# Performance work log

Hardware: AMD Instinct MI355X
Metric: run time of the kernel (lower is better)

## Reference

```python
import jax, jax.numpy as jnp
import numpy as np

B, T, C, H = 2, 512, 64, 64  # batch, seq (<= block_size), n_embd, head_size


def setup_inputs() -> dict:
    key = jax.random.key(0)
    ks = jax.random.split(key, 9)
    p = lambda k, sh: jax.random.normal(k, sh, jnp.float32) * 0.02
    return {
        "x": jax.random.normal(ks[0], (B, T, C), jnp.float32),
        "pos_emb": jax.random.normal(ks[1], (T, C), jnp.float32),
        "pos_dist_emb": jax.random.normal(ks[2], (B, T, T, 2 * C), jnp.float32),
        # GeluFeedForward(4c -> c -> 1): Linear(4c, c) -> GELU -> Linear(c, 1)
        "W1": p(ks[3], (4 * C, C)),
        "b1": p(ks[4], (C,)),
        "W2": p(ks[5], (C, 1)),
        "b2": p(ks[6], (1,)),
        # value projection Linear(c, head_size)
        "Wv": p(ks[7], (C, H)),
        "bv": p(ks[8], (H,)),
    }


def reference(x, pos_emb, pos_dist_emb, W1, b1, W2, b2, Wv, bv):
    b, t, c = x.shape
    x1 = x + pos_emb  # (b,t,c)
    # cat([k, q, pos_dist], -1) @ W1 == k@W1[:c] + q@W1[c:2c] + pd@W1[2c:]
    # (avoids materializing the (b,t,t,4c) repeat+cat tensor; same math)
    W1k, W1q, W1p = W1[:c], W1[c:2 * c], W1[2 * c:]
    kp = x1 @ W1k                 # (b,t,c): key side, varies over pair axis 2
    qp = x1 @ W1q                 # (b,t,c): query side, varies over pair axis 1
    pp = pos_dist_emb @ W1p       # (b,t,t,c)
    h = jax.nn.gelu(qp[:, :, None, :] + kp[:, None, :, :] + pp + b1,
                    approximate=False)          # (b,t,t,c)
    wei = ((h @ W2)[..., 0] + b2[0]) * (c ** -0.5)  # (b,t,t)
    causal = jnp.tril(jnp.ones((t, t), bool))
    wei = jnp.where(causal, wei, -jnp.inf)
    wei = jax.nn.softmax(wei, axis=-1)          # (b,t,t); dropout p=0
    v = x @ Wv + bv                             # (b,t,H)
    return wei @ v                              # (b,t,H)
```

## Files before the change

### kernel.cpp

```cpp
#include <hip/hip_runtime.h>
#include <math.h>

#define BB 2
#define TT 512
#define CC 64
#define HH 64
#define KK 128
#define PADK 136
#define JT 64

typedef __attribute__((ext_vector_type(8))) short short8;
typedef __attribute__((ext_vector_type(4))) float float4v;

__device__ inline unsigned short f2bf(float f) {
    unsigned int u = __float_as_uint(f);
    u = (u + 0x7FFFu + ((u >> 16) & 1u)) >> 16;
    return (unsigned short)u;
}

__global__ __launch_bounds__(256) void pack_kernel(
    const float* __restrict__ W1, unsigned short* __restrict__ Wpt)
{
    int t = blockIdx.x * 256 + threadIdx.x;
    int c = t >> 7;
    int k = t & 127;
    Wpt[c * PADK + k] = f2bf(W1[(2 * CC + k) * CC + c]);
}

__global__ __launch_bounds__(64) void prep_kernel(
    const float* __restrict__ x, const float* __restrict__ pos_emb,
    const float* __restrict__ W1, const float* __restrict__ b1,
    const float* __restrict__ Wv, const float* __restrict__ bv,
    float* __restrict__ kp, float* __restrict__ qpb, float* __restrict__ v)
{
    const int row = blockIdx.x;
    const int t = row & (TT - 1);
    const int c = threadIdx.x;
    __shared__ float xs[CC], x1s[CC];
    float xv = x[row * CC + c];
    xs[c] = xv;
    x1s[c] = xv + pos_emb[t * CC + c];
    __syncthreads();
    float ak = 0.f, aq = 0.f, av = 0.f;
#pragma unroll 8
    for (int k = 0; k < CC; ++k) {
        ak = fmaf(x1s[k], W1[k * CC + c], ak);
        aq = fmaf(x1s[k], W1[(CC + k) * CC + c], aq);
        av = fmaf(xs[k], Wv[k * HH + c], av);
    }
    kp[row * CC + c] = ak;
    qpb[row * CC + c] = aq + b1[c];
    v[row * HH + c] = av + bv[c];
}

__global__ __launch_bounds__(256) void wei_kernel(
    const float* __restrict__ pd, const unsigned short* __restrict__ Wpt,
    const float* __restrict__ W2, const float* __restrict__ b2,
    const float* __restrict__ kp, const float* __restrict__ qpb,
    float* __restrict__ wei)
{
    const int i = blockIdx.y;
    const int b = blockIdx.z;
    const int j0 = blockIdx.x * JT;
    if (j0 > i) return;

    __shared__ unsigned short Alds[JT * PADK];
    __shared__ unsigned short Blds[CC * PADK];

    const int tid = threadIdx.x;

    {
        const uint4* __restrict__ src = (const uint4*)Wpt;
        uint4* dst = (uint4*)Blds;
#pragma unroll
        for (int f = 0; f < 5; ++f) {
            int idx = f * 256 + tid;
            if (idx < (CC * PADK) / 8) dst[idx] = src[idx];
        }
    }

    {
        const float4* __restrict__ p4 =
            (const float4*)(pd + (((size_t)b * TT + i) * TT + j0) * KK);
#pragma unroll
        for (int it = 0; it < 8; ++it) {
            int f = it * 256 + tid;
            float4 val = p4[f];
            int j = f >> 5;
            int kq = f & 31;
            uint2 u;
            u.x = (unsigned)f2bf(val.x) | ((unsigned)f2bf(val.y) << 16);
            u.y = (unsigned)f2bf(val.z) | ((unsigned)f2bf(val.w) << 16);
            *(uint2*)&Alds[j * PADK + kq * 4] = u;
        }
    }
    __syncthreads();

    const int wave = tid >> 6;
    const int lane = tid & 63;
    const int m = lane & 15;
    const int kg = lane >> 4;

    float4v acc[4] = {{0.f,0.f,0.f,0.f},{0.f,0.f,0.f,0.f},
                      {0.f,0.f,0.f,0.f},{0.f,0.f,0.f,0.f}};
    const int arow = wave * 16 + m;
#pragma unroll
    for (int kt = 0; kt < 4; ++kt) {
        short8 a = *(const short8*)&Alds[arow * PADK + kt * 32 + kg * 8];
#pragma unroll
        for (int nt = 0; nt < 4; ++nt) {
            short8 bf = *(const short8*)&Blds[(nt * 16 + m) * PADK + kt * 32 + kg * 8];
            acc[nt] = __builtin_amdgcn_mfma_f32_16x16x32_bf16(a, bf, acc[nt], 0, 0, 0);
        }
    }

    float w2v[4], qv[4];
#pragma unroll
    for (int nt = 0; nt < 4; ++nt) {
        int c = nt * 16 + m;
        w2v[nt] = W2[c];
        qv[nt] = qpb[((size_t)b * TT + i) * CC + c];
    }
    const float b2v = b2[0];

#pragma unroll
    for (int r = 0; r < 4; ++r) {
        const int j = j0 + wave * 16 + kg * 4 + r;
        float s = 0.f;
#pragma unroll
        for (int nt = 0; nt < 4; ++nt) {
            float tv = acc[nt][r] + qv[nt] + kp[((size_t)b * TT + j) * CC + nt * 16 + m];
            float g = 0.5f * tv * (1.f + erff(tv * 0.70710678118654752f));
            s = fmaf(g, w2v[nt], s);
        }
#pragma unroll
        for (int off = 1; off < 16; off <<= 1) s += __shfl_xor(s, off);
        if (m == r && j <= i)
            wei[((size_t)b * TT + i) * TT + j] = (s + b2v) * 0.125f;
    }
}

__device__ inline float wave_reduce_max(float m) {
#pragma unroll
    for (int off = 32; off > 0; off >>= 1) m = fmaxf(m, __shfl_down(m, off));
    return m;
}
__device__ inline float wave_reduce_sum(float s) {
#pragma unroll
    for (int off = 32; off > 0; off >>= 1) s += __shfl_down(s, off);
    return s;
}

__global__ __launch_bounds__(256) void out_kernel(
    const float* __restrict__ wei, const float* __restrict__ v,
    float* __restrict__ out)
{
    const int i = blockIdx.x;
    const int b = blockIdx.y;
    const int tid = threadIdx.x;
    const int wv = tid >> 6;
    const int lane = tid & 63;
    const int n = i + 1;

    __shared__ float p[TT];
    __shared__ float red[4];
    __shared__ float part[4][HH];

    float m = -1e30f;
    for (int jj = tid; jj < n; jj += 256) {
        float w = wei[((size_t)b * TT + i) * TT + jj];
        p[jj] = w;
        m = fmaxf(m, w);
    }
    m = wave_reduce_max(m);
    if (lane == 0) red[wv] = m;
    __syncthreads();
    const float M = fmaxf(fmaxf(red[0], red[1]), fmaxf(red[2], red[3]));
    __syncthreads();

    float s = 0.f;
    for (int jj = tid; jj < n; jj += 256) {
        float e = __expf(p[jj] - M);
        p[jj] = e;
        s += e;
    }
    s = wave_reduce_sum(s);
    if (lane == 0) red[wv] = s;
    __syncthreads();
    const float S = red[0] + red[1] + red[2] + red[3];
    const float inv = 1.f / S;

    float acc = 0.f, acc2 = 0.f;
    int jj = wv;
    for (; jj + 4 < n; jj += 8) {
        acc  = fmaf(p[jj],     v[((size_t)b * TT + jj) * HH + lane], acc);
        acc2 = fmaf(p[jj + 4], v[((size_t)b * TT + jj + 4) * HH + lane], acc2);
    }
    if (jj < n)
        acc = fmaf(p[jj], v[((size_t)b * TT + jj) * HH + lane], acc);
    acc += acc2;
    part[wv][lane] = acc;
    __syncthreads();
    if (tid < HH) {
        float r = (part[0][tid] + part[1][tid] + part[2][tid] + part[3][tid]) * inv;
        out[((size_t)b * TT + i) * HH + tid] = r;
    }
}

extern "C" void kernel_launch(void* const* d_in, const int* in_sizes, int n_in,
                              void* d_out, int out_size, void* d_ws, size_t ws_size,
                              hipStream_t stream)
{
    const float* x       = (const float*)d_in[0];
    const float* pos_emb = (const float*)d_in[1];
    const float* pd      = (const float*)d_in[2];
    const float* W1      = (const float*)d_in[3];
    const float* b1      = (const float*)d_in[4];
    const float* W2      = (const float*)d_in[5];
    const float* b2      = (const float*)d_in[6];
    const float* Wv      = (const float*)d_in[7];
    const float* bv      = (const float*)d_in[8];
    float* out = (float*)d_out;

    float* ws = (float*)d_ws;
    unsigned short* Wpt = (unsigned short*)ws;
    float* kp  = ws + 4608;
    float* qpb = ws + 4608 + 65536;
    float* v   = ws + 4608 + 131072;
    float* wei = ws + 4608 + 196608;

    pack_kernel<<<dim3(32), dim3(256), 0, stream>>>(W1, Wpt);
    prep_kernel<<<dim3(BB * TT), dim3(64), 0, stream>>>(x, pos_emb, W1, b1, Wv, bv, kp, qpb, v);
    wei_kernel<<<dim3(TT / JT, TT, BB), dim3(256), 0, stream>>>(pd, Wpt, W2, b2, kp, qpb, wei);
    out_kernel<<<dim3(TT, BB), dim3(256), 0, stream>>>(wei, v, out);
}
```

Before: 405.4 us.

## Hold W1 fragments in registers, swizzle LDS, fuse weight packing into prep

The bf16 W1 slice is pre-packed in MFMA fragment order by extra blocks of prep_kernel, which removes the separate pack launch. wei_kernel then loads the B fragments directly into registers instead of staging them in LDS. This roughly halves shared memory per block, and launch bounds now request higher occupancy. The A tile drops its padding in favour of an XOR swizzle, kp values are prefetched before the barrier, and out_kernel accumulates with float4 loads and shuffle reductions. The trade-off is more register pressure from 16 short8 fragments plus kv values, which could cause spills under the tighter launch bounds.

```diff
diff --git a/kernel.cpp b/kernel.cpp
--- a/kernel.cpp
+++ b/kernel.cpp
@@ -6,7 +6,6 @@
 #define CC 64
 #define HH 64
 #define KK 128
-#define PADK 136
 #define JT 64
 
 typedef __attribute__((ext_vector_type(8))) short short8;
@@ -18,21 +17,30 @@
     return (unsigned short)u;
 }
 
-__global__ __launch_bounds__(256) void pack_kernel(
-    const float* __restrict__ W1, unsigned short* __restrict__ Wpt)
-{
-    int t = blockIdx.x * 256 + threadIdx.x;
-    int c = t >> 7;
-    int k = t & 127;
-    Wpt[c * PADK + k] = f2bf(W1[(2 * CC + k) * CC + c]);
-}
-
 __global__ __launch_bounds__(64) void prep_kernel(
     const float* __restrict__ x, const float* __restrict__ pos_emb,
     const float* __restrict__ W1, const float* __restrict__ b1,
     const float* __restrict__ Wv, const float* __restrict__ bv,
-    float* __restrict__ kp, float* __restrict__ qpb, float* __restrict__ v)
-{
+    float* __restrict__ kp, float* __restrict__ qpb, float* __restrict__ v,
+    unsigned short* __restrict__ Wpt)
+{
+    if (blockIdx.x >= BB * TT) {
+        int base = (blockIdx.x - BB * TT) * 256 + threadIdx.x;
+#pragma unroll
+        for (int q = 0; q < 4; ++q) {
+            int o  = base + q * 64;
+            int e  = o & 7;
+            int mm = (o >> 3) & 15;
+            int kg = (o >> 7) & 3;
+            int kt = (o >> 9) & 3;
+            int nt = (o >> 11) & 3;
+            int k = kt * 32 + kg * 8 + e;
+            int c = nt * 16 + mm;
+            Wpt[o] = f2bf(W1[(2 * CC + k) * CC + c]);
+        }
+        return;
+    }
+
     const int row = blockIdx.x;
     const int t = row & (TT - 1);
     const int c = threadIdx.x;
@@ -53,7 +61,7 @@
     v[row * HH + c] = av + bv[c];
 }
 
-__global__ __launch_bounds__(256) void wei_kernel(
+__global__ __launch_bounds__(256, 8) void wei_kernel(
     const float* __restrict__ pd, const unsigned short* __restrict__ Wpt,
     const float* __restrict__ W2, const float* __restrict__ b2,
     const float* __restrict__ kp, const float* __restrict__ qpb,
@@ -64,20 +72,36 @@
     const int j0 = blockIdx.x * JT;
     if (j0 > i) return;
 
-    __shared__ unsigned short Alds[JT * PADK];
-    __shared__ unsigned short Blds[CC * PADK];
-
-    const int tid = threadIdx.x;
-
-    {
-        const uint4* __restrict__ src = (const uint4*)Wpt;
-        uint4* dst = (uint4*)Blds;
-#pragma unroll
-        for (int f = 0; f < 5; ++f) {
-            int idx = f * 256 + tid;
-            if (idx < (CC * PADK) / 8) dst[idx] = src[idx];
-        }
-    }
+    __shared__ unsigned short Alds[JT * KK];
+
+    const int tid  = threadIdx.x;
+    const int wave = tid >> 6;
+    const int lane = tid & 63;
+    const int m    = lane & 15;
+    const int kg   = lane >> 4;
+
+    short8 bfrag[4][4];
+#pragma unroll
+    for (int nt = 0; nt < 4; ++nt)
+#pragma unroll
+        for (int kt = 0; kt < 4; ++kt)
+            bfrag[nt][kt] = *(const short8*)&Wpt[((nt * 4 + kt) * 64 + lane) * 8];
+
+    float w2v[4], qv[4], kv[4][4];
+#pragma unroll
+    for (int nt = 0; nt < 4; ++nt) {
+        int c = nt * 16 + m;
+        w2v[nt] = W2[c];
+        qv[nt]  = qpb[((size_t)b * TT + i) * CC + c];
+    }
+#pragma unroll
+    for (int r = 0; r < 4; ++r) {
+        int j = j0 + wave * 16 + kg * 4 + r;
+#pragma unroll
+        for (int nt = 0; nt < 4; ++nt)
+            kv[r][nt] = kp[((size_t)b * TT + j) * CC + nt * 16 + m];
+    }
+    const float b2v = b2[0];
 
     {
         const float4* __restrict__ p4 =
@@ -86,42 +110,28 @@
         for (int it = 0; it < 8; ++it) {
             int f = it * 256 + tid;
             float4 val = p4[f];
-            int j = f >> 5;
+            int j  = f >> 5;
             int kq = f & 31;
             uint2 u;
             u.x = (unsigned)f2bf(val.x) | ((unsigned)f2bf(val.y) << 16);
             u.y = (unsigned)f2bf(val.z) | ((unsigned)f2bf(val.w) << 16);
-            *(uint2*)&Alds[j * PADK + kq * 4] = u;
+            *(uint2*)&Alds[j * KK + ((kq * 4) ^ ((j & 7) << 3))] = u;
         }
     }
     __syncthreads();
-
-    const int wave = tid >> 6;
-    const int lane = tid & 63;
-    const int m = lane & 15;
-    const int kg = lane >> 4;
 
     float4v acc[4] = {{0.f,0.f,0.f,0.f},{0.f,0.f,0.f,0.f},
                       {0.f,0.f,0.f,0.f},{0.f,0.f,0.f,0.f}};
-    const int arow = wave * 16 + m;
+    const int arow  = wave * 16 + m;
+    const int abase = arow * KK;
+    const int a7    = (arow & 7) << 3;
 #pragma unroll
     for (int kt = 0; kt < 4; ++kt) {
-        short8 a = *(const short8*)&Alds[arow * PADK + kt * 32 + kg * 8];
-#pragma unroll
-        for (int nt = 0; nt < 4; ++nt) {
-            short8 bf = *(const short8*)&Blds[(nt * 16 + m) * PADK + kt * 32 + kg * 8];
-            acc[nt] = __builtin_amdgcn_mfma_f32_16x16x32_bf16(a, bf, acc[nt], 0, 0, 0);
-        }
-    }
-
-    float w2v[4], qv[4];
-#pragma unroll
-    for (int nt = 0; nt < 4; ++nt) {
-        int c = nt * 16 + m;
-        w2v[nt] = W2[c];
-        qv[nt] = qpb[((size_t)b * TT + i) * CC + c];
-    }
-    const float b2v = b2[0];
+        short8 a = *(const short8*)&Alds[abase + ((kt * 32 + kg * 8) ^ a7)];
+#pragma unroll
+        for (int nt = 0; nt < 4; ++nt)
+            acc[nt] = __builtin_amdgcn_mfma_f32_16x16x32_bf16(a, bfrag[nt][kt], acc[nt], 0, 0, 0);
+    }
 
 #pragma unroll
     for (int r = 0; r < 4; ++r) {
@@ -129,7 +139,7 @@
         float s = 0.f;
 #pragma unroll
         for (int nt = 0; nt < 4; ++nt) {
-            float tv = acc[nt][r] + qv[nt] + kp[((size_t)b * TT + j) * CC + nt * 16 + m];
+            float tv = acc[nt][r] + qv[nt] + kv[r][nt];
             float g = 0.5f * tv * (1.f + erff(tv * 0.70710678118654752f));
             s = fmaf(g, w2v[nt], s);
         }
@@ -164,16 +174,18 @@
 
     __shared__ float p[TT];
     __shared__ float red[4];
-    __shared__ float part[4][HH];
-
-    float m = -1e30f;
+    __shared__ float4v part[4][16];
+
+    const float* wrow = wei + ((size_t)b * TT + i) * TT;
+
+    float mx = -1e30f;
     for (int jj = tid; jj < n; jj += 256) {
-        float w = wei[((size_t)b * TT + i) * TT + jj];
+        float w = wrow[jj];
         p[jj] = w;
-        m = fmaxf(m, w);
-    }
-    m = wave_reduce_max(m);
-    if (lane == 0) red[wv] = m;
+        mx = fmaxf(mx, w);
+    }
+    mx = wave_reduce_max(mx);
+    if (lane == 0) red[wv] = mx;
     __syncthreads();
     const float M = fmaxf(fmaxf(red[0], red[1]), fmaxf(red[2], red[3]));
     __syncthreads();
@@ -190,20 +202,31 @@
     const float S = red[0] + red[1] + red[2] + red[3];
     const float inv = 1.f / S;
 
-    float acc = 0.f, acc2 = 0.f;
-    int jj = wv;
-    for (; jj + 4 < n; jj += 8) {
-        acc  = fmaf(p[jj],     v[((size_t)b * TT + jj) * HH + lane], acc);
-        acc2 = fmaf(p[jj + 4], v[((size_t)b * TT + jj + 4) * HH + lane], acc2);
-    }
-    if (jj < n)
-        acc = fmaf(p[jj], v[((size_t)b * TT + jj) * HH + lane], acc);
-    acc += acc2;
-    part[wv][lane] = acc;
-    __syncthreads();
-    if (tid < HH) {
-        float r = (part[0][tid] + part[1][tid] + part[2][tid] + part[3][tid]) * inv;
-        out[((size_t)b * TT + i) * HH + tid] = r;
+    const int c4 = lane & 15;
+    const int jr = lane >> 4;
+    const float4v* v4 = (const float4v*)(v + (size_t)b * TT * HH);
+    float4v acc = {0.f, 0.f, 0.f, 0.f};
+    for (int base = wv * 4; base < n; base += 16) {
+        int j = base + jr;
+        float pj = (j < n) ? p[j] : 0.f;
+        int jc = (j < n) ? j : 0;
+        float4v vv = v4[jc * 16 + c4];
+        acc += vv * pj;
+    }
+#pragma unroll
+    for (int off = 16; off <= 32; off <<= 1) {
+        float4v t;
+        t[0] = __shfl_xor(acc[0], off);
+        t[1] = __shfl_xor(acc[1], off);
+        t[2] = __shfl_xor(acc[2], off);
+        t[3] = __shfl_xor(acc[3], off);
+        acc += t;
+    }
+    if (jr == 0) part[wv][c4] = acc;
+    __syncthreads();
+    if (tid < 16) {
+        float4v r = (part[0][tid] + part[1][tid] + part[2][tid] + part[3][tid]) * inv;
+        *((float4v*)(out + ((size_t)b * TT + i) * HH) + tid) = r;
     }
 }
 
@@ -224,13 +247,12 @@
 
     float* ws = (float*)d_ws;
     unsigned short* Wpt = (unsigned short*)ws;
-    float* kp  = ws + 4608;
-    float* qpb = ws + 4608 + 65536;
-    float* v   = ws + 4608 + 131072;
-    float* wei = ws + 4608 + 196608;
-
-    pack_kernel<<<dim3(32), dim3(256), 0, stream>>>(W1, Wpt);
-    prep_kernel<<<dim3(BB * TT), dim3(64), 0, stream>>>(x, pos_emb, W1, b1, Wv, bv, kp, qpb, v);
+    float* kp  = ws + 4096;
+    float* qpb = ws + 4096 + 65536;
+    float* v   = ws + 4096 + 131072;
+    float* wei = ws + 4096 + 196608;
+
+    prep_kernel<<<dim3(BB * TT + 32), dim3(64), 0, stream>>>(x, pos_emb, W1, b1, Wv, bv, kp, qpb, v, Wpt);
     wei_kernel<<<dim3(TT / JT, TT, BB), dim3(256), 0, stream>>>(pd, Wpt, W2, b2, kp, qpb, wei);
     out_kernel<<<dim3(TT, BB), dim3(256), 0, stream>>>(wei, v, out);
 }
```

Result: slower. 489.9 us (+20.8%).
